# Kernel tuning notes

Hardware: AMD Instinct MI355X
Metric: run time of the kernel (lower is better)

## Reference

```python
import jax, jax.numpy as jnp
import numpy as np
import math

PHI = (1 + math.sqrt(5)) / 2
PI = math.pi
B, N, T, D, H = 2, 16, 512, 512, 8
DH = D // H
HALF = DH // 2
FF = int(D * PHI)  # 828
DC = D
PR_EPS = 1e-8
LN_EPS = 1e-5


def _ln(x, g, b):
    # x: (B,N,T,D); g,b: (N,D)
    mu = x.mean(axis=-1, keepdims=True)
    var = ((x - mu) ** 2).mean(axis=-1, keepdims=True)
    return (x - mu) * jax.lax.rsqrt(var + LN_EPS) * g[None, :, None, :] + b[None, :, None, :]


def _phase_resonance(a, b):
    # a, b: (B, N, D) in fp32; adjacent feature pairs = (re, im)
    pairs = a.shape[-1] // 2
    def to_phase(x):
        x2 = x.reshape(*x.shape[:-1], pairs, 2)
        return jnp.arctan2(x2[..., 1] + PR_EPS, x2[..., 0] + PR_EPS)
    ta, tb = to_phase(a), to_phase(b)
    delta = ta[..., :, None, :] - tb[..., None, :, :]  # (B, N, N, pairs)
    return jnp.cos(delta).mean(axis=-1)                # (B, N, N) in [-1, 1]


def setup_inputs():
    key = jax.random.key(0)
    ks = iter(jax.random.split(key, 24))
    w = lambda shape: jax.random.normal(next(ks), shape, jnp.float32) * 0.02
    return {
        'x': jax.random.normal(next(ks), (B, N, T, D), jnp.float32),
        'gate_w': w((N, D)),
        'gate_b': jnp.full((N,), 2.0, jnp.float32),  # torch init: bias=2.0
        'ln1_g': jnp.ones((N, D), jnp.float32),
        'ln1_b': jnp.zeros((N, D), jnp.float32),
        'wq': w((N, D, D)), 'wk': w((N, D, D)), 'wv': w((N, D, D)), 'wo': w((N, D, D)),
        'phase_angles': jnp.tile(jnp.linspace(0.0, PI, H, dtype=jnp.float32), (N, 1)),
        'ln2_g': jnp.ones((N, D), jnp.float32),
        'ln2_b': jnp.zeros((N, D), jnp.float32),
        'up_w': w((N, D, FF)), 'up_b': jnp.zeros((N, FF), jnp.float32),
        'down_w': w((N, FF, D)), 'down_b': jnp.zeros((N, D), jnp.float32),
        'commit_w': w((N, D)), 'commit_b': jnp.zeros((N,), jnp.float32),
        'center_w': w((N, D, DC)), 'center_b': jnp.zeros((N, DC), jnp.float32),
        'field_in_w': w((D, D)),
        'field_out_w': w((D, D)),
        'conductance': jnp.float32(1.0),
    }


def reference(x, gate_w, gate_b, ln1_g, ln1_b, wq, wk, wv, wo, phase_angles,
              ln2_g, ln2_b, up_w, up_b, down_w, down_b, commit_w, commit_b,
              center_w, center_b, field_in_w, field_out_w, conductance):
    # ---- BinaryAperture (straight-through binary gate) ----
    logits = jnp.einsum('bntd,nd->bnt', x, gate_w) + gate_b[None, :, None]
    prob = jax.nn.sigmoid(logits)  # temperature = 1.0
    hard = (prob > 0.5).astype(x.dtype)
    gate = (hard + prob - jax.lax.stop_gradient(prob))[..., None]  # (B,N,T,1)

    # ---- Field: phase-rotated, gated attention (scores forced to fp32) ----
    h = _ln(x, ln1_g, ln1_b)
    def proj(wm):
        z = jnp.einsum('bntd,nde->bnte', h, wm)
        return z.reshape(B, N, T, H, DH).transpose(0, 1, 3, 2, 4)  # (B,N,H,T,DH)
    Q, K, V = proj(wq), proj(wk), proj(wv)
    cos_a = jnp.cos(phase_angles)[None, :, :, None, None]  # (1,N,H,1,1)
    sin_a = jnp.sin(phase_angles)[None, :, :, None, None]
    def rot(Z):
        re, im = Z[..., :HALF], Z[..., HALF:2 * HALF]
        return jnp.concatenate([re * cos_a - im * sin_a, re * sin_a + im * cos_a], axis=-1)
    Q, K = rot(Q), rot(K)
    ge = gate[:, :, None]  # (B,N,1,T,1) broadcast over heads
    Q = Q * ge
    K = K * ge
    scores = jnp.einsum('bnhtd,bnhsd->bnhts', Q.astype(jnp.float32), K.astype(jnp.float32)) / math.sqrt(DH)
    attn = jax.nn.softmax(scores, axis=-1).astype(V.dtype)
    field = jnp.einsum('bnhts,bnhsd->bnhtd', attn, V)
    field = field.transpose(0, 1, 3, 2, 4).reshape(B, N, T, D)
    field = jnp.einsum('bntd,nde->bnte', field, wo) * gate
    x = x + field

    # ---- Boundary: golden-ratio FFN gated by commit * gate ----
    h2 = _ln(x, ln2_g, ln2_b)
    up = jax.nn.gelu(jnp.einsum('bntd,ndf->bntf', h2, up_w) + up_b[None, :, None], approximate=False)
    ff = jnp.einsum('bntf,nfd->bntd', up, down_w) + down_b[None, :, None]
    center_pool = x.mean(axis=2)  # (B,N,D) (pooled pre-FFN, as in torch)
    commit = jax.nn.sigmoid(jnp.einsum('bnd,nd->bn', center_pool, commit_w) + commit_b[None])  # (B,N)
    x = x + commit[..., None, None] * gate * ff
    center = jnp.tanh(jnp.einsum('bnd,nde->bne', center_pool, center_w) + center_b[None])  # (B,N,DC)

    # ---- SharedField: phase-resonance coupling across the N nodes ----
    node_gates = commit[..., None]  # (B,N,1)
    transmitted = center * node_gates
    h_res = jnp.einsum('bnd,de->bne', center, field_in_w).astype(jnp.float32)
    r_acc = _phase_resonance(h_res, h_res)  # (B,N,N); r_acc None -> r_acc_new = r_instant
    h_tx = jnp.einsum('bnd,de->bne', transmitted, field_in_w)
    recv = conductance * jnp.einsum('bmn,bnd->bmd', r_acc.astype(x.dtype), h_tx)
    field_signal = jnp.einsum('bnd,de->bne', recv, field_out_w)  # (B,N,D)

    # each node's boundary receives the field signal
    return x + field_signal[:, :, None, :]
```

## Files before the change

### kernel.cpp

```cpp
#include <hip/hip_runtime.h>

typedef unsigned short u16;
typedef __attribute__((ext_vector_type(8))) short short8;
typedef __attribute__((ext_vector_type(4))) float f32x4;

#define B_ 2
#define N_ 16
#define T_ 512
#define D_ 512
#define H_ 8
#define DH_ 64
#define HALF_ 32
#define FF_ 828
#define DC_ 512
#define LN_EPS 1e-5f
#define PR_EPS 1e-8f
#define NEG_INF (-3.0e38f)

__device__ __forceinline__ float b2f(u16 u) { return __uint_as_float(((unsigned)u) << 16); }
__device__ __forceinline__ u16 f2b(float f) {
  unsigned x = __float_as_uint(f);
  return (u16)((x + 0x7fffu + ((x >> 16) & 1u)) >> 16);
}
__device__ __forceinline__ float gelu_exact(float z) {
  return 0.5f * z * (1.f + erff(z * 0.70710678118654752f));
}

__global__ __launch_bounds__(256) void ln_gate_kernel(
    const float* __restrict__ xsrc,
    const float* __restrict__ gate_w, const float* __restrict__ gate_b,
    const float* __restrict__ lng, const float* __restrict__ lnb,
    float* __restrict__ gate_out, u16* __restrict__ h_out, int do_gate) {
  __shared__ float red[256];
  int bnt = blockIdx.x;
  int n = (bnt / T_) % N_;
  int tid = threadIdx.x;
  const float* xr = xsrc + (size_t)bnt * D_;
  float x0 = xr[tid], x1 = xr[tid + 256];
  red[tid] = x0 + x1; __syncthreads();
  for (int s = 128; s > 0; s >>= 1) { if (tid < s) red[tid] += red[tid + s]; __syncthreads(); }
  float mu = red[0] * (1.f / D_); __syncthreads();
  float d0 = x0 - mu, d1 = x1 - mu;
  red[tid] = d0 * d0 + d1 * d1; __syncthreads();
  for (int s = 128; s > 0; s >>= 1) { if (tid < s) red[tid] += red[tid + s]; __syncthreads(); }
  float rstd = rsqrtf(red[0] * (1.f / D_) + LN_EPS); __syncthreads();
  if (do_gate) {
    red[tid] = x0 * gate_w[n * D_ + tid] + x1 * gate_w[n * D_ + tid + 256];
    __syncthreads();
    for (int s = 128; s > 0; s >>= 1) { if (tid < s) red[tid] += red[tid + s]; __syncthreads(); }
    if (tid == 0) gate_out[bnt] = (red[0] + gate_b[n] > 0.f) ? 1.f : 0.f;
  }
  size_t o = (size_t)bnt * D_;
  h_out[o + tid]       = f2b(d0 * rstd * lng[n * D_ + tid]       + lnb[n * D_ + tid]);
  h_out[o + tid + 256] = f2b(d1 * rstd * lng[n * D_ + tid + 256] + lnb[n * D_ + tid + 256]);
}

#define BM 128
#define BN 128
#define BK 32
#define LST 40
__global__ __launch_bounds__(256) void gemm_mfma_kernel(
    const u16* __restrict__ In,
    const float* __restrict__ W0, const float* __restrict__ W1, const float* __restrict__ W2,
    u16* __restrict__ O0, u16* __restrict__ O1, u16* __restrict__ O2,
    float* __restrict__ OutF,
    int Kd, int E, int mode,
    const float* __restrict__ bias,
    const float* __restrict__ xres, const float* __restrict__ gate) {
  __shared__ u16 As[BM * LST];
  __shared__ u16 Bs[BN * LST];
  int z = blockIdx.z;
  int bn = z & 31, proj = z >> 5;
  int n = bn & (N_ - 1);
  const float* W = (proj == 0) ? W0 : ((proj == 1) ? W1 : W2);
  u16* Out = (proj == 0) ? O0 : ((proj == 1) ? O1 : O2);
  int e0 = blockIdx.x * BN, t0 = blockIdx.y * BM;
  int tid = threadIdx.x;
  int lane = tid & 63, wave = tid >> 6;
  int m_off = (wave & 1) * 64, n_off = (wave >> 1) * 64;
  int ml = lane & 15, quad = lane >> 4;
  const u16* Inb = In + (size_t)bn * T_ * Kd;
  const float* Wb = W + (size_t)n * Kd * E;

  f32x4 acc[4][4] = {};

  int ksteps = (Kd + BK - 1) / BK;
  for (int ks = 0; ks < ksteps; ++ks) {
    int k0 = ks * BK;
    #pragma unroll
    for (int it = 0; it < 2; ++it) {
      int slot = tid * 2 + it;
      int r = slot >> 2;
      int q = slot & 3;
      int kg = k0 + q * 8;
      const u16* src = Inb + (size_t)(t0 + r) * Kd + kg;
      u16* dst = &As[r * LST + q * 8];
      if (kg + 8 <= Kd) {
        *(ushort4*)(dst)     = *(const ushort4*)(src);
        *(ushort4*)(dst + 4) = *(const ushort4*)(src + 4);
      } else {
        #pragma unroll
        for (int xx = 0; xx < 8; ++xx) dst[xx] = (kg + xx < Kd) ? src[xx] : (u16)0;
      }
    }
    {
      int kk = tid & 31;
      int eb = (tid >> 5) * 16;
      int kg = k0 + kk;
      #pragma unroll
      for (int it = 0; it < 4; ++it) {
        int e = eb + it * 4;
        int eg = e0 + e;
        float4 w4 = {0.f, 0.f, 0.f, 0.f};
        if (kg < Kd && eg < E) w4 = *(const float4*)(Wb + (size_t)kg * E + eg);
        Bs[(e + 0) * LST + kk] = f2b(w4.x);
        Bs[(e + 1) * LST + kk] = f2b(w4.y);
        Bs[(e + 2) * LST + kk] = f2b(w4.z);
        Bs[(e + 3) * LST + kk] = f2b(w4.w);
      }
    }
    __syncthreads();
    short8 a[4], b[4];
    #pragma unroll
    for (int i = 0; i < 4; ++i)
      a[i] = *(const short8*)&As[(m_off + i * 16 + ml) * LST + quad * 8];
    #pragma unroll
    for (int j = 0; j < 4; ++j)
      b[j] = *(const short8*)&Bs[(n_off + j * 16 + ml) * LST + quad * 8];
    #pragma unroll
    for (int i = 0; i < 4; ++i)
      #pragma unroll
      for (int j = 0; j < 4; ++j)
        acc[i][j] = __builtin_amdgcn_mfma_f32_16x16x32_bf16(a[i], b[j], acc[i][j], 0, 0, 0);
    __syncthreads();
  }

  #pragma unroll
  for (int j = 0; j < 4; ++j) {
    int eg = e0 + n_off + j * 16 + ml;
    if (eg >= E) continue;
    #pragma unroll
    for (int i = 0; i < 4; ++i) {
      #pragma unroll
      for (int r = 0; r < 4; ++r) {
        int tg = t0 + m_off + i * 16 + quad * 4 + r;
        float v = acc[i][j][r];
        size_t o = (size_t)bn * T_ * E + (size_t)tg * E + eg;
        if (mode == 0) {
          Out[o] = f2b(v);
        } else if (mode == 1) {
          float g = gate[(size_t)bn * T_ + tg];
          OutF[o] = xres[o] + v * g;
        } else if (mode == 2) {
          Out[o] = f2b(gelu_exact(v + bias[(size_t)n * E + eg]));
        } else {
          Out[o] = f2b(v + bias[(size_t)n * E + eg]);
        }
      }
    }
  }
}

__global__ __launch_bounds__(256) void rot_gate_kernel(
    u16* __restrict__ q, u16* __restrict__ k,
    const float* __restrict__ phase, const float* __restrict__ gate) {
  long long i = (long long)blockIdx.x * 256 + threadIdx.x;
  int c = (int)(i & 31);
  int h = (int)((i >> 5) & 7);
  int t = (int)((i >> 8) & 511);
  int bn = (int)(i >> 17);
  int n = bn & (N_ - 1);
  float a = phase[n * H_ + h];
  float ca = cosf(a), sa = sinf(a);
  float g = gate[(size_t)bn * T_ + t];
  size_t base = ((size_t)bn * T_ + t) * D_ + h * DH_;
  float qr = b2f(q[base + c]), qi = b2f(q[base + c + HALF_]);
  q[base + c]         = f2b((qr * ca - qi * sa) * g);
  q[base + c + HALF_] = f2b((qr * sa + qi * ca) * g);
  float kr = b2f(k[base + c]), ki = b2f(k[base + c + HALF_]);
  k[base + c]         = f2b((kr * ca - ki * sa) * g);
  k[base + c + HALF_] = f2b((kr * sa + ki * ca) * g);
}

#define ATS 72
__global__ __launch_bounds__(256) void attn_kernel(
    const u16* __restrict__ Q, const u16* __restrict__ K, const u16* __restrict__ V,
    u16* __restrict__ O) {
  __shared__ __align__(16) u16 Qs[64 * ATS];
  __shared__ __align__(16) u16 Ks[64 * ATS];
  __shared__ __align__(16) u16 Vs[64 * ATS];
  __shared__ __align__(16) u16 Ps[64 * ATS];
  int qt = blockIdx.x, h = blockIdx.y, bn = blockIdx.z;
  int tid = threadIdx.x;
  int lane = tid & 63, wave = tid >> 6;
  int ml = lane & 15, quad = lane >> 4;
  int t0 = qt * 64;
  size_t rowbase = (size_t)bn * T_ * D_ + (size_t)h * DH_;

  {
    int r = tid >> 2;
    int c = (tid & 3) * 16;
    const u16* src = Q + rowbase + (size_t)(t0 + r) * D_ + c;
    #pragma unroll
    for (int hf = 0; hf < 2; ++hf) {
      short8 v = *(const short8*)(src + hf * 8);
      #pragma unroll
      for (int e = 0; e < 8; ++e)
        ((u16*)&v)[e] = f2b(b2f(((u16*)&v)[e]) * 0.125f);
      *(short8*)&Qs[r * ATS + c + hf * 8] = v;
    }
  }

  float m_[4], l_[4];
  f32x4 acco[4] = {};
  #pragma unroll
  for (int r = 0; r < 4; ++r) { m_[r] = NEG_INF; l_[r] = 0.f; }

  for (int sc = 0; sc < 8; ++sc) {
    int s0 = sc * 64;
    {
      int r = tid >> 2;
      int c = (tid & 3) * 16;
      const u16* src = K + rowbase + (size_t)(s0 + r) * D_ + c;
      *(short8*)&Ks[r * ATS + c]     = *(const short8*)(src);
      *(short8*)&Ks[r * ATS + c + 8] = *(const short8*)(src + 8);
    }
    {
      int sw = wave * 16;
      const u16* src = V + rowbase + (size_t)(s0 + sw) * D_ + lane;
      short8 v0, v1;
      #pragma unroll
      for (int r = 0; r < 8; ++r) ((u16*)&v0)[r] = src[(size_t)r * D_];
      #pragma unroll
      for (int r = 0; r < 8; ++r) ((u16*)&v1)[r] = src[(size_t)(r + 8) * D_];
      *(short8*)&Vs[lane * ATS + sw]     = v0;
      *(short8*)&Vs[lane * ATS + sw + 8] = v1;
    }
    __syncthreads();

    f32x4 s4[4] = {};
    #pragma unroll
    for (int kst = 0; kst < 2; ++kst) {
      short8 a = *(const short8*)&Qs[(wave * 16 + ml) * ATS + kst * 32 + quad * 8];
      #pragma unroll
      for (int j = 0; j < 4; ++j) {
        short8 b = *(const short8*)&Ks[(j * 16 + ml) * ATS + kst * 32 + quad * 8];
        s4[j] = __builtin_amdgcn_mfma_f32_16x16x32_bf16(a, b, s4[j], 0, 0, 0);
      }
    }

    #pragma unroll
    for (int r = 0; r < 4; ++r) {
      float cm = fmaxf(fmaxf(s4[0][r], s4[1][r]), fmaxf(s4[2][r], s4[3][r]));
      #pragma unroll
      for (int off = 1; off < 16; off <<= 1) cm = fmaxf(cm, __shfl_xor(cm, off));
      float mn = fmaxf(m_[r], cm);
      float al = expf(m_[r] - mn);
      u16 q0 = f2b(expf(s4[0][r] - mn)), q1 = f2b(expf(s4[1][r] - mn));
      u16 q2 = f2b(expf(s4[2][r] - mn)), q3 = f2b(expf(s4[3][r] - mn));
      float rs = b2f(q0) + b2f(q1) + b2f(q2) + b2f(q3);
      #pragma unroll
      for (int off = 1; off < 16; off <<= 1) rs += __shfl_xor(rs, off);
      l_[r] = l_[r] * al + rs;
      m_[r] = mn;
      #pragma unroll
      for (int jd = 0; jd < 4; ++jd) acco[jd][r] *= al;
      int trow = wave * 16 + quad * 4 + r;
      Ps[trow * ATS + 0 * 16 + ml] = q0;
      Ps[trow * ATS + 1 * 16 + ml] = q1;
      Ps[trow * ATS + 2 * 16 + ml] = q2;
      Ps[trow * ATS + 3 * 16 + ml] = q3;
    }

    #pragma unroll
    for (int sst = 0; sst < 2; ++sst) {
      short8 a = *(const short8*)&Ps[(wave * 16 + ml) * ATS + sst * 32 + quad * 8];
      #pragma unroll
      for (int jd = 0; jd < 4; ++jd) {
        short8 b = *(const short8*)&Vs[(jd * 16 + ml) * ATS + sst * 32 + quad * 8];
        acco[jd] = __builtin_amdgcn_mfma_f32_16x16x32_bf16(a, b, acco[jd], 0, 0, 0);
      }
    }
    __syncthreads();
  }

  #pragma unroll
  for (int r = 0; r < 4; ++r) {
    float inv = 1.f / l_[r];
    int trow = t0 + wave * 16 + quad * 4 + r;
    #pragma unroll
    for (int jd = 0; jd < 4; ++jd)
      O[rowbase + (size_t)trow * D_ + jd * 16 + ml] = f2b(acco[jd][r] * inv);
  }
}

__global__ __launch_bounds__(256) void pool_kernel(const float* __restrict__ x2, float* __restrict__ cp) {
  int bid = blockIdx.x;
  int bn = bid >> 1;
  int d = (bid & 1) * 256 + threadIdx.x;
  const float* base = x2 + (size_t)bn * T_ * D_ + d;
  float s = 0.f;
  for (int t = 0; t < T_; ++t) s += base[(size_t)t * D_];
  cp[(size_t)bn * D_ + d] = s * (1.f / T_);
}

__global__ __launch_bounds__(256) void commit_center_kernel(
    const float* __restrict__ cp, const float* __restrict__ commit_w, const float* __restrict__ commit_b,
    const float* __restrict__ center_w, const float* __restrict__ center_b,
    float* __restrict__ commit, float* __restrict__ center) {
  __shared__ float cps[512];
  __shared__ float red[256];
  int bn = blockIdx.x, n = bn % N_, tid = threadIdx.x;
  cps[tid] = cp[(size_t)bn * D_ + tid];
  cps[tid + 256] = cp[(size_t)bn * D_ + tid + 256];
  __syncthreads();
  red[tid] = cps[tid] * commit_w[n * D_ + tid] + cps[tid + 256] * commit_w[n * D_ + tid + 256];
  __syncthreads();
  for (int s = 128; s > 0; s >>= 1) { if (tid < s) red[tid] += red[tid + s]; __syncthreads(); }
  if (tid == 0) commit[bn] = 1.f / (1.f + expf(-(red[0] + commit_b[n])));
  #pragma unroll
  for (int eo = 0; eo < 2; ++eo) {
    int e = eo * 256 + tid;
    float acc = center_b[(size_t)n * DC_ + e];
    for (int d = 0; d < D_; ++d) acc = fmaf(cps[d], center_w[((size_t)n * D_ + d) * DC_ + e], acc);
    center[(size_t)bn * DC_ + e] = tanhf(acc);
  }
}

__global__ __launch_bounds__(256) void matvec_kernel(
    const float* __restrict__ inp, const float* __restrict__ Wm, float* __restrict__ outp) {
  __shared__ float s[512];
  int bn = blockIdx.x, tid = threadIdx.x;
  s[tid] = inp[(size_t)bn * D_ + tid];
  s[tid + 256] = inp[(size_t)bn * D_ + tid + 256];
  __syncthreads();
  #pragma unroll
  for (int eo = 0; eo < 2; ++eo) {
    int e = eo * 256 + tid;
    float acc = 0.f;
    for (int d = 0; d < D_; ++d) acc = fmaf(s[d], Wm[(size_t)d * D_ + e], acc);
    outp[(size_t)bn * D_ + e] = acc;
  }
}

__global__ __launch_bounds__(256) void uv_kernel(
    const float* __restrict__ hres, float* __restrict__ u, float* __restrict__ v) {
  int i = blockIdx.x * 256 + threadIdx.x;
  float xr = hres[2 * i] + PR_EPS;
  float yi = hres[2 * i + 1] + PR_EPS;
  float r = sqrtf(xr * xr + yi * yi);
  u[i] = xr / r; v[i] = yi / r;
}

__global__ __launch_bounds__(256) void racc_kernel(
    const float* __restrict__ u, const float* __restrict__ v, float* __restrict__ ra) {
  int b = blockIdx.x, tid = threadIdx.x;
  int mm = tid >> 4, nn = tid & 15;
  const float* ub = u + (size_t)b * N_ * 256;
  const float* vb = v + (size_t)b * N_ * 256;
  float acc = 0.f;
  for (int p = 0; p < 256; ++p)
    acc += ub[mm * 256 + p] * ub[nn * 256 + p] + vb[mm * 256 + p] * vb[nn * 256 + p];
  ra[(size_t)b * N_ * N_ + mm * N_ + nn] = acc * (1.f / 256.f);
}

__global__ __launch_bounds__(256) void recv_kernel(
    const float* __restrict__ ra, const float* __restrict__ commit,
    const float* __restrict__ hres, const float* __restrict__ cond, float* __restrict__ recv) {
  int bn = blockIdx.x, b = bn / N_, mm = bn % N_, tid = threadIdx.x;
  float c = cond[0];
  #pragma unroll
  for (int eo = 0; eo < 2; ++eo) {
    int d = eo * 256 + tid;
    float acc = 0.f;
    for (int nn = 0; nn < N_; ++nn)
      acc += ra[(size_t)b * N_ * N_ + mm * N_ + nn] * commit[b * N_ + nn] *
             hres[((size_t)b * N_ + nn) * D_ + d];
    recv[(size_t)bn * D_ + d] = c * acc;
  }
}

__global__ __launch_bounds__(256) void final_kernel(
    const float* __restrict__ x2, const float* __restrict__ commit,
    const float* __restrict__ gate, const u16* __restrict__ ff,
    const float* __restrict__ fs, float* __restrict__ out) {
  long long i4 = (long long)blockIdx.x * 256 + threadIdx.x;
  long long base = i4 * 4;
  int d = (int)(base & (D_ - 1));
  int t = (int)((base >> 9) & (T_ - 1));
  int bn = (int)(base >> 18);
  float cg = commit[bn] * gate[(size_t)bn * T_ + t];
  float4 xv = *(const float4*)(x2 + base);
  ushort4 fv = *(const ushort4*)(ff + base);
  float4 sv = *(const float4*)(fs + (size_t)bn * D_ + d);
  float4 r;
  r.x = xv.x + cg * b2f(fv.x) + sv.x;
  r.y = xv.y + cg * b2f(fv.y) + sv.y;
  r.z = xv.z + cg * b2f(fv.z) + sv.z;
  r.w = xv.w + cg * b2f(fv.w) + sv.w;
  *(float4*)(out + base) = r;
}

extern "C" void kernel_launch(void* const* d_in, const int* in_sizes, int n_in,
                              void* d_out, int out_size, void* d_ws, size_t ws_size,
                              hipStream_t stream) {
  (void)in_sizes; (void)n_in; (void)out_size; (void)ws_size;
  const float* x          = (const float*)d_in[0];
  const float* gate_w     = (const float*)d_in[1];
  const float* gate_b     = (const float*)d_in[2];
  const float* ln1_g      = (const float*)d_in[3];
  const float* ln1_b      = (const float*)d_in[4];
  const float* wq         = (const float*)d_in[5];
  const float* wk         = (const float*)d_in[6];
  const float* wv         = (const float*)d_in[7];
  const float* wo         = (const float*)d_in[8];
  const float* phase      = (const float*)d_in[9];
  const float* ln2_g      = (const float*)d_in[10];
  const float* ln2_b      = (const float*)d_in[11];
  const float* up_w       = (const float*)d_in[12];
  const float* up_b       = (const float*)d_in[13];
  const float* down_w     = (const float*)d_in[14];
  const float* down_b     = (const float*)d_in[15];
  const float* commit_w   = (const float*)d_in[16];
  const float* commit_b   = (const float*)d_in[17];
  const float* center_w   = (const float*)d_in[18];
  const float* center_b   = (const float*)d_in[19];
  const float* field_in_w = (const float*)d_in[20];
  const float* field_out_w= (const float*)d_in[21];
  const float* cond       = (const float*)d_in[22];

  const long long BNTD = 8388608LL;
  u16* w16 = (u16*)d_ws;
  u16* R0 = w16;
  u16* R1 = w16 + BNTD;
  u16* R2 = w16 + 2 * BNTD;
  u16* R3 = w16 + 3 * BNTD;
  float* sm   = (float*)(w16 + 4 * BNTD);
  float* gate   = sm;
  float* cp     = sm + 16384;
  float* center = sm + 2 * 16384;
  float* hres   = sm + 3 * 16384;
  float* uu     = sm + 4 * 16384;
  float* vv     = uu + 8192;
  float* ra     = vv + 8192;
  float* recvb  = ra + 512;
  float* fsig   = recvb + 16384;
  float* commit = fsig + 16384;
  float* x2 = (float*)d_out;

  ln_gate_kernel<<<16384, 256, 0, stream>>>(x, gate_w, gate_b, ln1_g, ln1_b, gate, R0, 1);
  gemm_mfma_kernel<<<dim3(4, 4, 96), 256, 0, stream>>>(
      R0, wq, wk, wv, R1, R2, R3, nullptr, 512, 512, 0, nullptr, nullptr, nullptr);
  rot_gate_kernel<<<16384, 256, 0, stream>>>(R1, R2, phase, gate);
  attn_kernel<<<dim3(8, 8, 32), 256, 0, stream>>>(R1, R2, R3, R0);
  gemm_mfma_kernel<<<dim3(4, 4, 32), 256, 0, stream>>>(
      R0, wo, nullptr, nullptr, nullptr, nullptr, nullptr, x2, 512, 512, 1, nullptr, x, gate);
  ln_gate_kernel<<<16384, 256, 0, stream>>>(x2, nullptr, nullptr, ln2_g, ln2_b, nullptr, R1, 0);
  gemm_mfma_kernel<<<dim3(7, 4, 32), 256, 0, stream>>>(
      R1, up_w, nullptr, nullptr, R2, nullptr, nullptr, nullptr, 512, 828, 2, up_b, nullptr, nullptr);
  gemm_mfma_kernel<<<dim3(4, 4, 32), 256, 0, stream>>>(
      R2, down_w, nullptr, nullptr, R0, nullptr, nullptr, nullptr, 828, 512, 3, down_b, nullptr, nullptr);
  pool_kernel<<<64, 256, 0, stream>>>(x2, cp);
  commit_center_kernel<<<32, 256, 0, stream>>>(cp, commit_w, commit_b, center_w, center_b, commit, center);
  matvec_kernel<<<32, 256, 0, stream>>>(center, field_in_w, hres);
  uv_kernel<<<32, 256, 0, stream>>>(hres, uu, vv);
  racc_kernel<<<2, 256, 0, stream>>>(uu, vv, ra);
  recv_kernel<<<32, 256, 0, stream>>>(ra, commit, hres, cond, recvb);
  matvec_kernel<<<32, 256, 0, stream>>>(recvb, field_out_w, fsig);
  final_kernel<<<8192, 256, 0, stream>>>(x2, commit, gate, R0, fsig, x2);
}
```

Before: 917.6 us.

## Pre-transpose weights to bf16 once per call for vectorized GEMM B-tile loads

```diff
diff --git a/kernel.cpp b/kernel.cpp
--- a/kernel.cpp
+++ b/kernel.cpp
@@ -55,6 +55,46 @@
   h_out[o + tid + 256] = f2b(d1 * rstd * lng[n * D_ + tid + 256] + lnb[n * D_ + tid + 256]);
 }
 
+__global__ __launch_bounds__(256) void wconv_kernel(
+    const float* __restrict__ W, u16* __restrict__ Wt, int Kd, int E) {
+  __shared__ u16 tile[32][33];
+  int e0 = blockIdx.x * 32, k0 = blockIdx.y * 32, n = blockIdx.z;
+  const float* Wb = W + (size_t)n * Kd * E;
+  u16* Wtb = Wt + (size_t)n * E * Kd;
+  int r = threadIdx.x >> 3, c4 = (threadIdx.x & 7) * 4;
+  int kk = k0 + r;
+  if (kk < Kd) {
+    if (e0 + c4 + 3 < E) {
+      float4 w4 = *(const float4*)(Wb + (size_t)kk * E + e0 + c4);
+      tile[r][c4 + 0] = f2b(w4.x); tile[r][c4 + 1] = f2b(w4.y);
+      tile[r][c4 + 2] = f2b(w4.z); tile[r][c4 + 3] = f2b(w4.w);
+    } else {
+      #pragma unroll
+      for (int j = 0; j < 4; ++j) {
+        int ee = e0 + c4 + j;
+        tile[r][c4 + j] = (ee < E) ? f2b(Wb[(size_t)kk * E + ee]) : (u16)0;
+      }
+    }
+  } else {
+    #pragma unroll
+    for (int j = 0; j < 4; ++j) tile[r][c4 + j] = 0;
+  }
+  __syncthreads();
+  int ee = e0 + r;
+  if (ee < E) {
+    u16* dst = Wtb + (size_t)ee * Kd + k0 + c4;
+    if (k0 + c4 + 3 < Kd) {
+      ushort4 o;
+      o.x = tile[c4 + 0][r]; o.y = tile[c4 + 1][r];
+      o.z = tile[c4 + 2][r]; o.w = tile[c4 + 3][r];
+      *(ushort4*)dst = o;
+    } else {
+      #pragma unroll
+      for (int j = 0; j < 4; ++j) if (k0 + c4 + j < Kd) dst[j] = tile[c4 + j][r];
+    }
+  }
+}
+
 #define BM 128
 #define BN 128
 #define BK 32
@@ -62,6 +102,7 @@
 __global__ __launch_bounds__(256) void gemm_mfma_kernel(
     const u16* __restrict__ In,
     const float* __restrict__ W0, const float* __restrict__ W1, const float* __restrict__ W2,
+    const u16* __restrict__ Wt0, const u16* __restrict__ Wt1, const u16* __restrict__ Wt2,
     u16* __restrict__ O0, u16* __restrict__ O1, u16* __restrict__ O2,
     float* __restrict__ OutF,
     int Kd, int E, int mode,
@@ -73,6 +114,7 @@
   int bn = z & 31, proj = z >> 5;
   int n = bn & (N_ - 1);
   const float* W = (proj == 0) ? W0 : ((proj == 1) ? W1 : W2);
+  const u16* Wt = (proj == 0) ? Wt0 : ((proj == 1) ? Wt1 : Wt2);
   u16* Out = (proj == 0) ? O0 : ((proj == 1) ? O1 : O2);
   int e0 = blockIdx.x * BN, t0 = blockIdx.y * BM;
   int tid = threadIdx.x;
@@ -80,7 +122,8 @@
   int m_off = (wave & 1) * 64, n_off = (wave >> 1) * 64;
   int ml = lane & 15, quad = lane >> 4;
   const u16* Inb = In + (size_t)bn * T_ * Kd;
-  const float* Wb = W + (size_t)n * Kd * E;
+  const float* Wb = W ? W + (size_t)n * Kd * E : nullptr;
+  const u16* Wtb = Wt ? Wt + (size_t)n * E * Kd : nullptr;
 
   f32x4 acc[4][4] = {};
 
@@ -103,7 +146,24 @@
         for (int xx = 0; xx < 8; ++xx) dst[xx] = (kg + xx < Kd) ? src[xx] : (u16)0;
       }
     }
-    {
+    if (Wtb) {
+      #pragma unroll
+      for (int it = 0; it < 2; ++it) {
+        int slot = tid * 2 + it;
+        int r = slot >> 2;
+        int q = slot & 3;
+        int kg = k0 + q * 8;
+        const u16* src = Wtb + (size_t)(e0 + r) * Kd + kg;
+        u16* dst = &Bs[r * LST + q * 8];
+        if (kg + 8 <= Kd) {
+          *(ushort4*)(dst)     = *(const ushort4*)(src);
+          *(ushort4*)(dst + 4) = *(const ushort4*)(src + 4);
+        } else {
+          #pragma unroll
+          for (int xx = 0; xx < 8; ++xx) dst[xx] = (kg + xx < Kd) ? src[xx] : (u16)0;
+        }
+      }
+    } else {
       int kk = tid & 31;
       int eb = (tid >> 5) * 16;
       int kg = k0 + kk;
@@ -404,7 +464,7 @@
 extern "C" void kernel_launch(void* const* d_in, const int* in_sizes, int n_in,
                               void* d_out, int out_size, void* d_ws, size_t ws_size,
                               hipStream_t stream) {
-  (void)in_sizes; (void)n_in; (void)out_size; (void)ws_size;
+  (void)in_sizes; (void)n_in; (void)out_size;
   const float* x          = (const float*)d_in[0];
   const float* gate_w     = (const float*)d_in[1];
   const float* gate_b     = (const float*)d_in[2];
@@ -448,18 +508,49 @@
   float* commit = fsig + 16384;
   float* x2 = (float*)d_out;
 
+  const size_t WSQ = (size_t)N_ * 512 * 512;
+  const size_t WUP = (size_t)N_ * 512 * 828;
+  u16* wtbase = (u16*)(sm + 115232);
+  u16* wtq = wtbase;
+  u16* wtk = wtq + WSQ;
+  u16* wtv = wtk + WSQ;
+  u16* wto = wtv + WSQ;
+  u16* wtu = wto + WSQ;
+  u16* wtd = wtu + WUP;
+  size_t needed = (size_t)((char*)(wtd + WUP) - (char*)d_ws);
+  bool use_wt = ws_size >= needed;
+
   ln_gate_kernel<<<16384, 256, 0, stream>>>(x, gate_w, gate_b, ln1_g, ln1_b, gate, R0, 1);
+
+  if (use_wt) {
+    wconv_kernel<<<dim3(16, 16, 16), 256, 0, stream>>>(wq, wtq, 512, 512);
+    wconv_kernel<<<dim3(16, 16, 16), 256, 0, stream>>>(wk, wtk, 512, 512);
+    wconv_kernel<<<dim3(16, 16, 16), 256, 0, stream>>>(wv, wtv, 512, 512);
+    wconv_kernel<<<dim3(16, 16, 16), 256, 0, stream>>>(wo, wto, 512, 512);
+    wconv_kernel<<<dim3(26, 16, 16), 256, 0, stream>>>(up_w, wtu, 512, 828);
+    wconv_kernel<<<dim3(16, 26, 16), 256, 0, stream>>>(down_w, wtd, 828, 512);
+  }
+  const u16* pq = use_wt ? wtq : nullptr;
+  const u16* pk = use_wt ? wtk : nullptr;
+  const u16* pv = use_wt ? wtv : nullptr;
+  const u16* po = use_wt ? wto : nullptr;
+  const u16* pu = use_wt ? wtu : nullptr;
+  const u16* pd = use_wt ? wtd : nullptr;
+
   gemm_mfma_kernel<<<dim3(4, 4, 96), 256, 0, stream>>>(
-      R0, wq, wk, wv, R1, R2, R3, nullptr, 512, 512, 0, nullptr, nullptr, nullptr);
+      R0, wq, wk, wv, pq, pk, pv, R1, R2, R3, nullptr, 512, 512, 0, nullptr, nullptr, nullptr);
   rot_gate_kernel<<<16384, 256, 0, stream>>>(R1, R2, phase, gate);
   attn_kernel<<<dim3(8, 8, 32), 256, 0, stream>>>(R1, R2, R3, R0);
   gemm_mfma_kernel<<<dim3(4, 4, 32), 256, 0, stream>>>(
-      R0, wo, nullptr, nullptr, nullptr, nullptr, nullptr, x2, 512, 512, 1, nullptr, x, gate);
+      R0, wo, nullptr, nullptr, po, nullptr, nullptr, nullptr, nullptr, nullptr, x2,
+      512, 512, 1, nullptr, x, gate);
   ln_gate_kernel<<<16384, 256, 0, stream>>>(x2, nullptr, nullptr, ln2_g, ln2_b, nullptr, R1, 0);
   gemm_mfma_kernel<<<dim3(7, 4, 32), 256, 0, stream>>>(
-      R1, up_w, nullptr, nullptr, R2, nullptr, nullptr, nullptr, 512, 828, 2, up_b, nullptr, nullptr);
+      R1, up_w, nullptr, nullptr, pu, nullptr, nullptr, R2, nullptr, nullptr, nullptr,
+      512, 828, 2, up_b, nullptr, nullptr);
   gemm_mfma_kernel<<<dim3(4, 4, 32), 256, 0, stream>>>(
-      R2, down_w, nullptr, nullptr, R0, nullptr, nullptr, nullptr, 828, 512, 3, down_b, nullptr, nullptr);
+      R2, down_w, nullptr, nullptr, pd, nullptr, nullptr, R0, nullptr, nullptr, nullptr,
+      828, 512, 3, down_b, nullptr, nullptr);
   pool_kernel<<<64, 256, 0, stream>>>(x2, cp);
   commit_center_kernel<<<32, 256, 0, stream>>>(cp, commit_w, commit_b, center_w, center_b, commit, center);
   matvec_kernel<<<32, 256, 0, stream>>>(center, field_in_w, hres);
```

New measurement: 886.2 us. 1.04x faster.
